# Performance work log

Measured on AMD Instinct MI355X. Metric: run time of the kernel, lower is better.

## Reference

```python
import jax, jax.numpy as jnp
import numpy as np

N_NODES = 50000
N_EDGES = 1000000
NODE_DIM = 128
EDGE_DIM = 64


def setup_inputs() -> dict:
    key = jax.random.key(0)
    ks = jax.random.split(key, 12)
    s = 1.0 / np.sqrt(EDGE_DIM)
    sn = 1.0 / np.sqrt(NODE_DIM)
    return {
        "x": jax.random.normal(ks[0], (N_NODES, NODE_DIM), jnp.float32),
        "edge_index": jax.random.randint(ks[1], (2, N_EDGES), 0, N_NODES, jnp.int64),
        "edge_attr": jax.random.normal(ks[2], (N_EDGES, EDGE_DIM), jnp.float32),
        # lin_e: edge_dim -> edge_dim
        "We": jax.random.uniform(ks[3], (EDGE_DIM, EDGE_DIM), jnp.float32, -s, s),
        "be": jax.random.uniform(ks[4], (EDGE_DIM,), jnp.float32, -s, s),
        # lin_s: node_dim -> edge_dim
        "Ws": jax.random.uniform(ks[5], (EDGE_DIM, NODE_DIM), jnp.float32, -sn, sn),
        "bs": jax.random.uniform(ks[6], (EDGE_DIM,), jnp.float32, -sn, sn),
        # lin_t: node_dim -> edge_dim
        "Wt": jax.random.uniform(ks[7], (EDGE_DIM, NODE_DIM), jnp.float32, -sn, sn),
        "bt": jax.random.uniform(ks[8], (EDGE_DIM,), jnp.float32, -sn, sn),
        # lin1: edge_dim -> edge_dim
        "W1": jax.random.uniform(ks[9], (EDGE_DIM, EDGE_DIM), jnp.float32, -s, s),
        "b1": jax.random.uniform(ks[10], (EDGE_DIM,), jnp.float32, -s, s),
    }


def reference(x, edge_index, edge_attr, We, be, Ws, bs, Wt, bt, W1, b1):
    # node projections: [N, edge_dim]
    x_s = x @ Ws.T + bs
    x_t = x @ Wt.T + bt
    # fused edge update: lin_e(edge_attr) + gather(x_s, src) + gather(x_t, tgt)
    e = edge_attr @ We.T + be + x_s[edge_index[0]] + x_t[edge_index[1]]  # [E, edge_dim]
    e = jax.nn.gelu(e)
    return e @ W1.T + b1
```

## Files before the change

### kernel.cpp

```cpp
#include <hip/hip_runtime.h>
#include <stdint.h>

#define N_NODES_C 50000
#define N_EDGES_C 1000000
#define NODE_DIM_C 128
#define EDGE_DIM_C 64

typedef __attribute__((ext_vector_type(8))) short short8;
typedef __attribute__((ext_vector_type(4))) float floatx4;

__device__ __forceinline__ short f2bf(float f) {
    union { float f; uint32_t u; } v; v.f = f;
    uint32_t u = v.u;
    uint32_t r = (u + 0x7FFFu + ((u >> 16) & 1u)) >> 16;
    return (short)r;
}

__device__ __forceinline__ short8 pack8(float4 a0, float4 a1) {
    short8 o;
    o[0] = f2bf(a0.x); o[1] = f2bf(a0.y); o[2] = f2bf(a0.z); o[3] = f2bf(a0.w);
    o[4] = f2bf(a1.x); o[5] = f2bf(a1.y); o[6] = f2bf(a1.z); o[7] = f2bf(a1.w);
    return o;
}

__device__ __forceinline__ float gelu_tanh(float x) {
    float u = x * x;
    float inner = x * (1.0f + 0.044715f * u);
    float z = 1.5957691216057308f * inner;
    float ez = __expf(-z);
    return x / (1.0f + ez);
}

__global__ __launch_bounds__(256) void node_proj_kernel(
    const float* __restrict__ x,
    const float* __restrict__ Ws, const float* __restrict__ bs,
    const float* __restrict__ Wt, const float* __restrict__ bt,
    float* __restrict__ xs, float* __restrict__ xt)
{
    __shared__ __align__(16) short ws_frag[4][4][64][8];
    __shared__ __align__(16) short wt_frag[4][4][64][8];

    const int tid = threadIdx.x;
    const int wave = tid >> 6, lane = tid & 63;
    const int m = lane & 15, q = lane >> 4;
    const int base = blockIdx.x * 64 + wave * 16;
    const int arow = base + m;

    float4 av[4][2];
#pragma unroll
    for (int s = 0; s < 4; ++s) {
        if (arow < N_NODES_C) {
            const float4* ap = (const float4*)(x + arow * NODE_DIM_C + s * 32 + q * 8);
            av[s][0] = ap[0]; av[s][1] = ap[1];
        } else {
            av[s][0] = make_float4(0.f, 0.f, 0.f, 0.f);
            av[s][1] = make_float4(0.f, 0.f, 0.f, 0.f);
        }
    }

    for (int eidx = tid; eidx < 1024; eidx += 256) {
        int t = eidx >> 8;
        int s = (eidx >> 6) & 3;
        int l = eidx & 63;
        int n = t * 16 + (l & 15);
        int kb = s * 32 + ((l >> 4) << 3);
        const float4* wsr = (const float4*)(Ws + n * NODE_DIM_C + kb);
        const float4* wtr = (const float4*)(Wt + n * NODE_DIM_C + kb);
        float4 s0 = wsr[0], s1 = wsr[1];
        float4 t0 = wtr[0], t1 = wtr[1];
        *(short8*)ws_frag[t][s][l] = pack8(s0, s1);
        *(short8*)wt_frag[t][s][l] = pack8(t0, t1);
    }
    __syncthreads();

    floatx4 accS[4], accT[4];
    const floatx4 zero = {0.f, 0.f, 0.f, 0.f};
#pragma unroll
    for (int t = 0; t < 4; ++t) { accS[t] = zero; accT[t] = zero; }

#pragma unroll
    for (int s = 0; s < 4; ++s) {
        short8 a = pack8(av[s][0], av[s][1]);
#pragma unroll
        for (int t = 0; t < 4; ++t) {
            short8 bS = *(const short8*)ws_frag[t][s][lane];
            short8 bT = *(const short8*)wt_frag[t][s][lane];
            accS[t] = __builtin_amdgcn_mfma_f32_16x16x32_bf16(a, bS, accS[t], 0, 0, 0);
            accT[t] = __builtin_amdgcn_mfma_f32_16x16x32_bf16(a, bT, accT[t], 0, 0, 0);
        }
    }

#pragma unroll
    for (int t = 0; t < 4; ++t) {
        int col = t * 16 + m;
        float bsv = bs[col], btv = bt[col];
#pragma unroll
        for (int r = 0; r < 4; ++r) {
            int n = base + q * 4 + r;
            if (n < N_NODES_C) {
                xs[n * EDGE_DIM_C + col] = accS[t][r] + bsv;
                xt[n * EDGE_DIM_C + col] = accT[t][r] + btv;
            }
        }
    }
}

__global__ __launch_bounds__(256) void edge_mlp_kernel(
    const float* __restrict__ ea, const int* __restrict__ ei,
    const float* __restrict__ We, const float* __restrict__ be,
    const float* __restrict__ W1, const float* __restrict__ b1,
    const float* __restrict__ xs, const float* __restrict__ xt,
    float* __restrict__ out)
{
    __shared__ __align__(16) short we_frag[4][2][64][8];
    __shared__ __align__(16) short w1_frag[4][2][64][8];
    __shared__ __align__(16) short pbuf[4][16][72];

    const int tid = threadIdx.x;
    const int wave = tid >> 6, lane = tid & 63;
    const int m = lane & 15, q = lane >> 4;
    const int base = blockIdx.x * 64 + wave * 16;
    const int* __restrict__ src = ei;
    const int* __restrict__ tgt = ei + N_EDGES_C;

    int sidx[4], tidx[4];
#pragma unroll
    for (int r = 0; r < 4; ++r) {
        int e = base + q * 4 + r;
        int si = src[e], ti = tgt[e];
        sidx[r] = min(max(si, 0), N_NODES_C - 1);
        tidx[r] = min(max(ti, 0), N_NODES_C - 1);
    }

    float4 av[4];
#pragma unroll
    for (int s = 0; s < 2; ++s) {
        const float4* ap = (const float4*)(ea + (base + m) * EDGE_DIM_C + s * 32 + q * 8);
        av[s * 2] = ap[0];
        av[s * 2 + 1] = ap[1];
    }

    float4 web[2][2], w1b[2][2];
#pragma unroll
    for (int j = 0; j < 2; ++j) {
        int eidx = tid + j * 256;
        int t = eidx >> 7, s = (eidx >> 6) & 1, l = eidx & 63;
        int n = t * 16 + (l & 15);
        int kb = s * 32 + ((l >> 4) << 3);
        const float4* wer = (const float4*)(We + n * EDGE_DIM_C + kb);
        const float4* w1r = (const float4*)(W1 + n * EDGE_DIM_C + kb);
        web[j][0] = wer[0]; web[j][1] = wer[1];
        w1b[j][0] = w1r[0]; w1b[j][1] = w1r[1];
    }

    float bev[4], b1v[4];
#pragma unroll
    for (int t = 0; t < 4; ++t) { bev[t] = be[t * 16 + m]; b1v[t] = b1[t * 16 + m]; }

    float gxs[4][4], gxt[4][4];
#pragma unroll
    for (int r = 0; r < 4; ++r) {
        const float* ps = xs + (size_t)sidx[r] * EDGE_DIM_C + m;
        const float* pt = xt + (size_t)tidx[r] * EDGE_DIM_C + m;
#pragma unroll
        for (int t = 0; t < 4; ++t) {
            gxs[r][t] = ps[t * 16];
            gxt[r][t] = pt[t * 16];
        }
    }

#pragma unroll
    for (int j = 0; j < 2; ++j) {
        int eidx = tid + j * 256;
        int t = eidx >> 7, s = (eidx >> 6) & 1, l = eidx & 63;
        *(short8*)we_frag[t][s][l] = pack8(web[j][0], web[j][1]);
        *(short8*)w1_frag[t][s][l] = pack8(w1b[j][0], w1b[j][1]);
    }

    short8 af[2];
#pragma unroll
    for (int s = 0; s < 2; ++s) af[s] = pack8(av[s * 2], av[s * 2 + 1]);

    __syncthreads();

    const floatx4 zero = {0.f, 0.f, 0.f, 0.f};
    floatx4 acc[4];
#pragma unroll
    for (int t = 0; t < 4; ++t) acc[t] = zero;
#pragma unroll
    for (int s = 0; s < 2; ++s) {
#pragma unroll
        for (int t = 0; t < 4; ++t) {
            short8 b = *(const short8*)we_frag[t][s][lane];
            acc[t] = __builtin_amdgcn_mfma_f32_16x16x32_bf16(af[s], b, acc[t], 0, 0, 0);
        }
    }

#pragma unroll
    for (int t = 0; t < 4; ++t) {
#pragma unroll
        for (int r = 0; r < 4; ++r) {
            float c = acc[t][r] + bev[t] + gxs[r][t] + gxt[r][t];
            pbuf[wave][q * 4 + r][t * 16 + m] = f2bf(gelu_tanh(c));
        }
    }

    floatx4 acc2[4];
#pragma unroll
    for (int t = 0; t < 4; ++t) acc2[t] = zero;
#pragma unroll
    for (int s = 0; s < 2; ++s) {
        short8 a2 = *(const short8*)&pbuf[wave][m][s * 32 + q * 8];
#pragma unroll
        for (int t = 0; t < 4; ++t) {
            short8 b = *(const short8*)w1_frag[t][s][lane];
            acc2[t] = __builtin_amdgcn_mfma_f32_16x16x32_bf16(a2, b, acc2[t], 0, 0, 0);
        }
    }

#pragma unroll
    for (int t = 0; t < 4; ++t) {
        int col = t * 16 + m;
#pragma unroll
        for (int r = 0; r < 4; ++r) {
            int e = base + q * 4 + r;
            out[e * EDGE_DIM_C + col] = acc2[t][r] + b1v[t];
        }
    }
}

extern "C" void kernel_launch(void* const* d_in, const int* in_sizes, int n_in,
                              void* d_out, int out_size, void* d_ws, size_t ws_size,
                              hipStream_t stream) {
    const float* x   = (const float*)d_in[0];
    const int*   ei  = (const int*)d_in[1];
    const float* ea  = (const float*)d_in[2];
    const float* We  = (const float*)d_in[3];
    const float* be  = (const float*)d_in[4];
    const float* Ws  = (const float*)d_in[5];
    const float* bs  = (const float*)d_in[6];
    const float* Wt  = (const float*)d_in[7];
    const float* bt  = (const float*)d_in[8];
    const float* W1  = (const float*)d_in[9];
    const float* b1  = (const float*)d_in[10];
    float* out = (float*)d_out;

    float* xs = (float*)d_ws;
    float* xt = xs + (size_t)N_NODES_C * EDGE_DIM_C;

    dim3 blk(256);
    dim3 grid_nodes((N_NODES_C + 63) / 64);
    node_proj_kernel<<<grid_nodes, blk, 0, stream>>>(x, Ws, bs, Wt, bt, xs, xt);

    dim3 grid_edges(N_EDGES_C / 64);
    edge_mlp_kernel<<<grid_edges, blk, 0, stream>>>(ea, ei, We, be, W1, b1, xs, xt, out);
}
```

Baseline: 531.7 us.

## Make edge kernel persistent over five chunks with prefetched gathers and permuted node layout

The edge kernel now runs 3125 blocks, each looping over five strided 64-edge chunks. Each iteration prefetches the next chunk's edge_attr and indices (two ahead for indices) and issues the next node-feature gathers while the current MLP runs. The node projection stores its outputs in a permuted layout so each lane gathers one float4 per edge instead of four scalar loads. Per-block weight staging is amortized over five chunks. In exchange, register pressure rises and fewer blocks are in flight.

```diff
diff --git a/kernel.cpp b/kernel.cpp
--- a/kernel.cpp
+++ b/kernel.cpp
@@ -21,6 +21,10 @@
     o[0] = f2bf(a0.x); o[1] = f2bf(a0.y); o[2] = f2bf(a0.z); o[3] = f2bf(a0.w);
     o[4] = f2bf(a1.x); o[5] = f2bf(a1.y); o[6] = f2bf(a1.z); o[7] = f2bf(a1.w);
     return o;
+}
+
+__device__ __forceinline__ float f4get(const float4& v, int t) {
+    return t == 0 ? v.x : t == 1 ? v.y : t == 2 ? v.z : v.w;
 }
 
 __device__ __forceinline__ float gelu_tanh(float x) {
@@ -35,7 +39,7 @@
     const float* __restrict__ x,
     const float* __restrict__ Ws, const float* __restrict__ bs,
     const float* __restrict__ Wt, const float* __restrict__ bt,
-    float* __restrict__ xs, float* __restrict__ xt)
+    float* __restrict__ xsp, float* __restrict__ xtp)
 {
     __shared__ __align__(16) short ws_frag[4][4][64][8];
     __shared__ __align__(16) short wt_frag[4][4][64][8];
@@ -71,6 +75,11 @@
         *(short8*)ws_frag[t][s][l] = pack8(s0, s1);
         *(short8*)wt_frag[t][s][l] = pack8(t0, t1);
     }
+
+    float bsv[4], btv[4];
+#pragma unroll
+    for (int t = 0; t < 4; ++t) { bsv[t] = bs[t * 16 + m]; btv[t] = bt[t * 16 + m]; }
+
     __syncthreads();
 
     floatx4 accS[4], accT[4];
@@ -91,16 +100,15 @@
     }
 
 #pragma unroll
-    for (int t = 0; t < 4; ++t) {
-        int col = t * 16 + m;
-        float bsv = bs[col], btv = bt[col];
-#pragma unroll
-        for (int r = 0; r < 4; ++r) {
-            int n = base + q * 4 + r;
-            if (n < N_NODES_C) {
-                xs[n * EDGE_DIM_C + col] = accS[t][r] + bsv;
-                xt[n * EDGE_DIM_C + col] = accT[t][r] + btv;
-            }
+    for (int r = 0; r < 4; ++r) {
+        int n = base + q * 4 + r;
+        if (n < N_NODES_C) {
+            float4 vs = make_float4(accS[0][r] + bsv[0], accS[1][r] + bsv[1],
+                                    accS[2][r] + bsv[2], accS[3][r] + bsv[3]);
+            float4 vt = make_float4(accT[0][r] + btv[0], accT[1][r] + btv[1],
+                                    accT[2][r] + btv[2], accT[3][r] + btv[3]);
+            *(float4*)(xsp + n * EDGE_DIM_C + m * 4) = vs;
+            *(float4*)(xtp + n * EDGE_DIM_C + m * 4) = vt;
         }
     }
 }
@@ -109,7 +117,7 @@
     const float* __restrict__ ea, const int* __restrict__ ei,
     const float* __restrict__ We, const float* __restrict__ be,
     const float* __restrict__ W1, const float* __restrict__ b1,
-    const float* __restrict__ xs, const float* __restrict__ xt,
+    const float* __restrict__ xsp, const float* __restrict__ xtp,
     float* __restrict__ out)
 {
     __shared__ __align__(16) short we_frag[4][2][64][8];
@@ -119,25 +127,22 @@
     const int tid = threadIdx.x;
     const int wave = tid >> 6, lane = tid & 63;
     const int m = lane & 15, q = lane >> 4;
-    const int base = blockIdx.x * 64 + wave * 16;
     const int* __restrict__ src = ei;
     const int* __restrict__ tgt = ei + N_EDGES_C;
 
-    int sidx[4], tidx[4];
-#pragma unroll
-    for (int r = 0; r < 4; ++r) {
-        int e = base + q * 4 + r;
-        int si = src[e], ti = tgt[e];
-        sidx[r] = min(max(si, 0), N_NODES_C - 1);
-        tidx[r] = min(max(ti, 0), N_NODES_C - 1);
-    }
-
-    float4 av[4];
-#pragma unroll
-    for (int s = 0; s < 2; ++s) {
-        const float4* ap = (const float4*)(ea + (base + m) * EDGE_DIM_C + s * 32 + q * 8);
-        av[s * 2] = ap[0];
-        av[s * 2 + 1] = ap[1];
+    const int G = 3125;
+    const int cstride = G * 64;
+    const int cb0 = blockIdx.x * 64 + wave * 16;
+
+    int4 sI[2], tI[2];
+    sI[0] = *(const int4*)(src + cb0 + q * 4);
+    tI[0] = *(const int4*)(tgt + cb0 + q * 4);
+
+    float4 eab[4];
+    {
+        const float4* ap = (const float4*)(ea + (cb0 + m) * EDGE_DIM_C);
+        eab[0] = ap[q * 2];     eab[1] = ap[q * 2 + 1];
+        eab[2] = ap[8 + q * 2]; eab[3] = ap[8 + q * 2 + 1];
     }
 
     float4 web[2][2], w1b[2][2];
@@ -153,21 +158,12 @@
         w1b[j][0] = w1r[0]; w1b[j][1] = w1r[1];
     }
 
+    sI[1] = *(const int4*)(src + cb0 + cstride + q * 4);
+    tI[1] = *(const int4*)(tgt + cb0 + cstride + q * 4);
+
     float bev[4], b1v[4];
 #pragma unroll
     for (int t = 0; t < 4; ++t) { bev[t] = be[t * 16 + m]; b1v[t] = b1[t * 16 + m]; }
-
-    float gxs[4][4], gxt[4][4];
-#pragma unroll
-    for (int r = 0; r < 4; ++r) {
-        const float* ps = xs + (size_t)sidx[r] * EDGE_DIM_C + m;
-        const float* pt = xt + (size_t)tidx[r] * EDGE_DIM_C + m;
-#pragma unroll
-        for (int t = 0; t < 4; ++t) {
-            gxs[r][t] = ps[t * 16];
-            gxt[r][t] = pt[t * 16];
-        }
-    }
 
 #pragma unroll
     for (int j = 0; j < 2; ++j) {
@@ -176,55 +172,111 @@
         *(short8*)we_frag[t][s][l] = pack8(web[j][0], web[j][1]);
         *(short8*)w1_frag[t][s][l] = pack8(w1b[j][0], w1b[j][1]);
     }
-
-    short8 af[2];
-#pragma unroll
-    for (int s = 0; s < 2; ++s) af[s] = pack8(av[s * 2], av[s * 2 + 1]);
-
     __syncthreads();
 
+    float4 g_s[4], g_t[4];
+    {
+        int s0 = min(max(sI[0].x, 0), N_NODES_C - 1);
+        int s1 = min(max(sI[0].y, 0), N_NODES_C - 1);
+        int s2 = min(max(sI[0].z, 0), N_NODES_C - 1);
+        int s3 = min(max(sI[0].w, 0), N_NODES_C - 1);
+        int t0 = min(max(tI[0].x, 0), N_NODES_C - 1);
+        int t1 = min(max(tI[0].y, 0), N_NODES_C - 1);
+        int t2 = min(max(tI[0].z, 0), N_NODES_C - 1);
+        int t3 = min(max(tI[0].w, 0), N_NODES_C - 1);
+        g_s[0] = *(const float4*)(xsp + (s0 << 6) + m * 4);
+        g_s[1] = *(const float4*)(xsp + (s1 << 6) + m * 4);
+        g_s[2] = *(const float4*)(xsp + (s2 << 6) + m * 4);
+        g_s[3] = *(const float4*)(xsp + (s3 << 6) + m * 4);
+        g_t[0] = *(const float4*)(xtp + (t0 << 6) + m * 4);
+        g_t[1] = *(const float4*)(xtp + (t1 << 6) + m * 4);
+        g_t[2] = *(const float4*)(xtp + (t2 << 6) + m * 4);
+        g_t[3] = *(const float4*)(xtp + (t3 << 6) + m * 4);
+    }
+
     const floatx4 zero = {0.f, 0.f, 0.f, 0.f};
-    floatx4 acc[4];
-#pragma unroll
-    for (int t = 0; t < 4; ++t) acc[t] = zero;
-#pragma unroll
-    for (int s = 0; s < 2; ++s) {
-#pragma unroll
-        for (int t = 0; t < 4; ++t) {
-            short8 b = *(const short8*)we_frag[t][s][lane];
-            acc[t] = __builtin_amdgcn_mfma_f32_16x16x32_bf16(af[s], b, acc[t], 0, 0, 0);
-        }
-    }
-
-#pragma unroll
-    for (int t = 0; t < 4; ++t) {
-#pragma unroll
-        for (int r = 0; r < 4; ++r) {
-            float c = acc[t][r] + bev[t] + gxs[r][t] + gxt[r][t];
-            pbuf[wave][q * 4 + r][t * 16 + m] = f2bf(gelu_tanh(c));
-        }
-    }
-
-    floatx4 acc2[4];
-#pragma unroll
-    for (int t = 0; t < 4; ++t) acc2[t] = zero;
-#pragma unroll
-    for (int s = 0; s < 2; ++s) {
-        short8 a2 = *(const short8*)&pbuf[wave][m][s * 32 + q * 8];
-#pragma unroll
-        for (int t = 0; t < 4; ++t) {
-            short8 b = *(const short8*)w1_frag[t][s][lane];
-            acc2[t] = __builtin_amdgcn_mfma_f32_16x16x32_bf16(a2, b, acc2[t], 0, 0, 0);
-        }
-    }
-
-#pragma unroll
-    for (int t = 0; t < 4; ++t) {
-        int col = t * 16 + m;
-#pragma unroll
-        for (int r = 0; r < 4; ++r) {
-            int e = base + q * 4 + r;
-            out[e * EDGE_DIM_C + col] = acc2[t][r] + b1v[t];
+
+#pragma unroll
+    for (int k = 0; k < 5; ++k) {
+        short8 af0 = pack8(eab[0], eab[1]);
+        short8 af1 = pack8(eab[2], eab[3]);
+
+        if (k < 4) {
+            const float4* ap = (const float4*)(ea + (cb0 + (k + 1) * cstride + m) * EDGE_DIM_C);
+            eab[0] = ap[q * 2];     eab[1] = ap[q * 2 + 1];
+            eab[2] = ap[8 + q * 2]; eab[3] = ap[8 + q * 2 + 1];
+        }
+        if (k < 3) {
+            int b2 = cb0 + (k + 2) * cstride + q * 4;
+            sI[k & 1] = *(const int4*)(src + b2);
+            tI[k & 1] = *(const int4*)(tgt + b2);
+        }
+
+        floatx4 acc[4];
+#pragma unroll
+        for (int t = 0; t < 4; ++t) acc[t] = zero;
+#pragma unroll
+        for (int t = 0; t < 4; ++t) {
+            short8 b = *(const short8*)we_frag[t][0][lane];
+            acc[t] = __builtin_amdgcn_mfma_f32_16x16x32_bf16(af0, b, acc[t], 0, 0, 0);
+        }
+#pragma unroll
+        for (int t = 0; t < 4; ++t) {
+            short8 b = *(const short8*)we_frag[t][1][lane];
+            acc[t] = __builtin_amdgcn_mfma_f32_16x16x32_bf16(af1, b, acc[t], 0, 0, 0);
+        }
+
+#pragma unroll
+        for (int t = 0; t < 4; ++t) {
+#pragma unroll
+            for (int r = 0; r < 4; ++r) {
+                float c = acc[t][r] + bev[t] + f4get(g_s[r], t) + f4get(g_t[r], t);
+                pbuf[wave][q * 4 + r][t * 16 + m] = f2bf(gelu_tanh(c));
+            }
+        }
+
+        if (k < 4) {
+            int4 s4 = sI[(k + 1) & 1], t4 = tI[(k + 1) & 1];
+            int s0 = min(max(s4.x, 0), N_NODES_C - 1);
+            int s1 = min(max(s4.y, 0), N_NODES_C - 1);
+            int s2 = min(max(s4.z, 0), N_NODES_C - 1);
+            int s3 = min(max(s4.w, 0), N_NODES_C - 1);
+            int t0 = min(max(t4.x, 0), N_NODES_C - 1);
+            int t1 = min(max(t4.y, 0), N_NODES_C - 1);
+            int t2 = min(max(t4.z, 0), N_NODES_C - 1);
+            int t3 = min(max(t4.w, 0), N_NODES_C - 1);
+            g_s[0] = *(const float4*)(xsp + (s0 << 6) + m * 4);
+            g_s[1] = *(const float4*)(xsp + (s1 << 6) + m * 4);
+            g_s[2] = *(const float4*)(xsp + (s2 << 6) + m * 4);
+            g_s[3] = *(const float4*)(xsp + (s3 << 6) + m * 4);
+            g_t[0] = *(const float4*)(xtp + (t0 << 6) + m * 4);
+            g_t[1] = *(const float4*)(xtp + (t1 << 6) + m * 4);
+            g_t[2] = *(const float4*)(xtp + (t2 << 6) + m * 4);
+            g_t[3] = *(const float4*)(xtp + (t3 << 6) + m * 4);
+        }
+
+        floatx4 acc2[4];
+#pragma unroll
+        for (int t = 0; t < 4; ++t) acc2[t] = zero;
+#pragma unroll
+        for (int s = 0; s < 2; ++s) {
+            short8 a2 = *(const short8*)&pbuf[wave][m][s * 32 + q * 8];
+#pragma unroll
+            for (int t = 0; t < 4; ++t) {
+                short8 b = *(const short8*)w1_frag[t][s][lane];
+                acc2[t] = __builtin_amdgcn_mfma_f32_16x16x32_bf16(a2, b, acc2[t], 0, 0, 0);
+            }
+        }
+
+        const int ebase = cb0 + k * cstride;
+#pragma unroll
+        for (int t = 0; t < 4; ++t) {
+            int col = t * 16 + m;
+#pragma unroll
+            for (int r = 0; r < 4; ++r) {
+                int e = ebase + q * 4 + r;
+                out[e * EDGE_DIM_C + col] = acc2[t][r] + b1v[t];
+            }
         }
     }
 }
@@ -245,13 +297,13 @@
     const float* b1  = (const float*)d_in[10];
     float* out = (float*)d_out;
 
-    float* xs = (float*)d_ws;
-    float* xt = xs + (size_t)N_NODES_C * EDGE_DIM_C;
+    float* xsp = (float*)d_ws;
+    float* xtp = xsp + (size_t)N_NODES_C * EDGE_DIM_C;
 
     dim3 blk(256);
     dim3 grid_nodes((N_NODES_C + 63) / 64);
-    node_proj_kernel<<<grid_nodes, blk, 0, stream>>>(x, Ws, bs, Wt, bt, xs, xt);
-
-    dim3 grid_edges(N_EDGES_C / 64);
-    edge_mlp_kernel<<<grid_edges, blk, 0, stream>>>(ea, ei, We, be, W1, b1, xs, xt, out);
-}
+    node_proj_kernel<<<grid_nodes, blk, 0, stream>>>(x, Ws, bs, Wt, bt, xsp, xtp);
+
+    dim3 grid_edges(3125);
+    edge_mlp_kernel<<<grid_edges, blk, 0, stream>>>(ea, ei, We, be, W1, b1, xsp, xtp, out);
+}
```

Result: faster. 508.2 us (-4.4%).
